# Kernel optimization log

Hardware: AMD Instinct MI355X
Metric: run time of the kernel (lower is better)

Reference implementation:

```python
import jax, jax.numpy as jnp
import numpy as np

RATIOS = np.array([0.5, 1.0, 2.0], np.float32)
SCALES = np.array([8.0, 16.0, 32.0], np.float32)
IMAGE_SIZE = 1920.0
UPPER, LOWER = 0.4, 0.1
NPOS_MAX, NNEG_MAX = 128, 60   # sample_num=256 -> bg_num = min(60, 256-npos) = 60
BETA = 0.1
EPS = 1e-6


def make_anchors(H, W, stride):
    # K = len(RATIOS)*len(SCALES) anchors per grid cell, sizes stride*scale, aspect per ratio
    ws = (stride * SCALES[None, :] * np.sqrt(1.0 / RATIOS[:, None])).reshape(-1)  # [K]
    hs = (stride * SCALES[None, :] * np.sqrt(RATIOS[:, None])).reshape(-1)        # [K]
    cx = (np.arange(W, dtype=np.float32) + 0.5) * stride
    cy = (np.arange(H, dtype=np.float32) + 0.5) * stride
    cxg, cyg = np.meshgrid(cx, cy)  # [H, W]
    a = np.stack([cxg[..., None] - ws / 2, cyg[..., None] - hs / 2,
                  cxg[..., None] + ws / 2, cyg[..., None] + hs / 2], axis=-1)  # [H, W, K, 4]
    return jnp.asarray(a, jnp.float32)


def pairwise_iou(b, g):
    # b: [A, 4], g: [M, 4] -> [A, M]
    ab = jnp.maximum(b[:, 2] - b[:, 0], 0.0) * jnp.maximum(b[:, 3] - b[:, 1], 0.0)
    ag = jnp.maximum(g[:, 2] - g[:, 0], 0.0) * jnp.maximum(g[:, 3] - g[:, 1], 0.0)
    x1 = jnp.maximum(b[:, None, 0], g[None, :, 0])
    y1 = jnp.maximum(b[:, None, 1], g[None, :, 1])
    x2 = jnp.minimum(b[:, None, 2], g[None, :, 2])
    y2 = jnp.minimum(b[:, None, 3], g[None, :, 3])
    inter = jnp.maximum(x2 - x1, 0.0) * jnp.maximum(y2 - y1, 0.0)
    return inter / (ab[:, None] + ag[None, :] - inter + EPS)


def encode(box, anchor):
    # standard (tx, ty, tw, th) box encoding relative to anchor
    aw = anchor[:, 2] - anchor[:, 0]; ah = anchor[:, 3] - anchor[:, 1]
    acx = anchor[:, 0] + 0.5 * aw; acy = anchor[:, 1] + 0.5 * ah
    bw = jnp.maximum(box[:, 2] - box[:, 0], EPS); bh = jnp.maximum(box[:, 3] - box[:, 1], EPS)
    bcx = box[:, 0] + 0.5 * bw; bcy = box[:, 1] + 0.5 * bh
    return jnp.stack([(bcx - acx) / aw, (bcy - acy) / ah,
                      jnp.log(bw / aw), jnp.log(bh / ah)], axis=-1)


def smooth_l1(d):
    ad = jnp.abs(d)
    return jnp.where(ad < BETA, 0.5 * d * d / BETA, ad - 0.5 * BETA)


def per_image(regions, cls, gt, key, anchors_flat, n_norm):
    iou = pairwise_iou(regions, gt)                       # [A, M]
    best = iou.max(axis=1)
    arg = iou.argmax(axis=1).astype(jnp.int32)
    # match(): >= upper -> gt index (positive), < lower -> NEGATIVE(-1), else ignore(-2)
    matches = jnp.where(best >= UPPER, arg, jnp.where(best < LOWER, -1, -2))
    kp, kn = jax.random.split(key)
    # randperm-style sampling without replacement: top_k over random scores on masked anchors
    pos_score = jnp.where(matches >= 0, jax.random.uniform(kp, matches.shape), -1.0)
    pv, pidx = jax.lax.top_k(pos_score, NPOS_MAX)
    pvalid = (pv > 0.0).astype(jnp.float32)               # npos = min(num_pos, 128)
    neg_score = jnp.where(matches == -1, jax.random.uniform(kn, matches.shape), -1.0)
    nv, nidx = jax.lax.top_k(neg_score, NNEG_MAX)
    nvalid = (nv > 0.0).astype(jnp.float32)
    npos = pvalid.sum(); nneg = nvalid.sum()
    lp = cls[pidx]; ln = cls[nidx]
    # BCEWithLogits(mean): label 1 -> softplus(-x), label 0 -> softplus(x)
    bce = jnp.sum(jax.nn.softplus(-lp) * pvalid) + jnp.sum(jax.nn.softplus(ln) * nvalid)
    denom = jnp.maximum(npos + nneg, 1.0)
    cls_loss = bce / denom
    gt_sel = gt[jnp.clip(matches[pidx], 0, gt.shape[0] - 1)]
    anc = anchors_flat[pidx]
    tp = encode(regions[pidx], anc)
    tg = encode(gt_sel, anc)
    l1 = smooth_l1(tp - tg).sum(-1)                       # [NPOS_MAX]
    bbox_loss = jnp.sum(l1 * pvalid) / (jnp.maximum(npos, 1.0) * n_norm)
    pred_mean = (jnp.sum(lp * pvalid) + jnp.sum(ln * nvalid)) / denom
    return cls_loss, bbox_loss, npos, nneg, pred_mean


def reference(cls_scores, bbox_deltas, gt_boxes):
    N, K, H, W = cls_scores.shape
    stride = round(IMAGE_SIZE / W)
    anc = make_anchors(H, W, stride)                      # [H, W, K, 4]
    deltas = bbox_deltas.transpose(0, 2, 3, 1).reshape(N, H, W, K, 4)
    # regions = anchors + deltas, cross_boundary(remove=False) -> clip to image
    regions = jnp.clip(anc[None] + deltas, 0.0, IMAGE_SIZE).reshape(N, -1, 4)
    cls = cls_scores.transpose(0, 2, 3, 1).reshape(N, -1)
    keys = jax.random.split(jax.random.key(42), N)
    cl, bl, fg, bg, pm = jax.vmap(per_image, in_axes=(0, 0, 0, 0, None, None))(
        regions, cls, gt_boxes, keys, anc.reshape(-1, 4), float(N))
    return (cl.sum(), bl.sum(), bg.sum(), fg.sum(), pm[-1])


def setup_inputs():
    key = jax.random.key(0)
    k1, k2, k3, k4 = jax.random.split(key, 4)
    N, K, H, W, M = 8, 9, 120, 120, 64
    cls_scores = jax.random.normal(k1, (N, K, H, W), jnp.float32)
    bbox_deltas = jax.random.normal(k2, (N, 4 * K, H, W), jnp.float32) * 4.0
    xy = jax.random.uniform(k3, (N, M, 2), jnp.float32) * 1500.0
    wh = jax.random.uniform(k4, (N, M, 2), jnp.float32) * 360.0 + 40.0
    gt_boxes = jnp.concatenate([xy, xy + wh], axis=-1)    # valid [x1,y1,x2,y2] in-image
    return {"cls_scores": cls_scores, "bbox_deltas": bbox_deltas, "gt_boxes": gt_boxes}
```

## Files before the change

kernel.cpp:

```cpp
#include <hip/hip_runtime.h>
#include <stdint.h>

#define N_IMG 8
#define K_ANC 9
#define HW_G  14400
#define W_G   120
#define A_TOT 129600
#define M_GT  64
#define NBIN  1024
#define CAP   2048
#define WIN_TOT 2025
#define WPB   4
#define NBLK_M 507
#define NSUB2 64

#define POISON_U32 0xAAAAAAAAu

static constexpr size_t OFF_PHIST = 0;
static constexpr size_t OFF_NHIST = 32768;
static constexpr size_t OFF_CNT   = 65536;
static constexpr size_t OFF_THR   = 65600;
static constexpr size_t OFF_DONE_M= 65792;
static constexpr size_t OFF_DONE  = 65856;
static constexpr size_t OFF_DONE_F= 65888;
static constexpr size_t OFF_ACC   = 65920;
static constexpr size_t OFF_ENT   = 67584;
static constexpr size_t OFF_BND   = OFF_ENT + 4ull * N_IMG * A_TOT;

__device__ __forceinline__ uint32_t rotl32(uint32_t v, int r) {
  return (v << r) | (v >> (32 - r));
}

__device__ void tf2x32(uint32_t k0, uint32_t k1, uint32_t x0, uint32_t x1,
                       uint32_t& o0, uint32_t& o1) {
  uint32_t ks2 = 0x1BD11BDAu ^ k0 ^ k1;
  x0 += k0; x1 += k1;
#define TF_R(r) { x0 += x1; x1 = rotl32(x1, r); x1 ^= x0; }
  TF_R(13) TF_R(15) TF_R(26) TF_R(6)
  x0 += k1; x1 += ks2 + 1u;
  TF_R(17) TF_R(29) TF_R(16) TF_R(24)
  x0 += ks2; x1 += k0 + 2u;
  TF_R(13) TF_R(15) TF_R(26) TF_R(6)
  x0 += k0; x1 += k1 + 3u;
  TF_R(17) TF_R(29) TF_R(16) TF_R(24)
  x0 += k1; x1 += ks2 + 4u;
  TF_R(13) TF_R(15) TF_R(26) TF_R(6)
  x0 += ks2; x1 += k0 + 5u;
#undef TF_R
  o0 = x0; o1 = x1;
}

constexpr uint64_t tf_c(uint32_t k0, uint32_t k1, uint32_t x0, uint32_t x1) {
  const int R[20] = {13,15,26,6,17,29,16,24,13,15,26,6,17,29,16,24,13,15,26,6};
  uint32_t ks[3] = {k0, k1, 0x1BD11BDAu ^ k0 ^ k1};
  x0 += k0; x1 += k1;
  for (int r = 0; r < 20; ++r) {
    x0 += x1; x1 = (x1 << R[r]) | (x1 >> (32 - R[r])); x1 ^= x0;
    if ((r & 3) == 3) {
      int d = r / 4 + 1;
      x0 += ks[d % 3]; x1 += ks[(d + 1) % 3] + (uint32_t)d;
    }
  }
  return ((uint64_t)x0 << 32) | x1;
}

struct KeyTab { uint32_t v[N_IMG][4]; };
constexpr KeyTab make_keys() {
  KeyTab K{};
  for (int n = 0; n < N_IMG; ++n) {
    uint64_t f = tf_c(0u, 42u, 0u, (uint32_t)n);
    uint32_t i0 = (uint32_t)(f >> 32), i1 = (uint32_t)f;
    uint64_t p = tf_c(i0, i1, 0u, 0u);
    uint64_t q = tf_c(i0, i1, 0u, 1u);
    K.v[n][0] = (uint32_t)(p >> 32); K.v[n][1] = (uint32_t)p;
    K.v[n][2] = (uint32_t)(q >> 32); K.v[n][3] = (uint32_t)q;
  }
  return K;
}
__constant__ KeyTab KEYS = make_keys();

__device__ __forceinline__ float rlanef(float v, int l) {
  return __int_as_float(__builtin_amdgcn_readlane(__float_as_int(v), l));
}

__device__ void acc_pos(int n, int l, int m, const float* __restrict__ cls,
                        const float* __restrict__ del, const float* __restrict__ gt,
                        float& sp, float& pr, float& l1s) {
  int k = l / HW_G, hw = l - k * HW_G;
  const float scales[3] = {8.f, 16.f, 32.f};
  const float ratios[3] = {0.5f, 1.f, 2.f};
  float sc = scales[k % 3], rt = ratios[k / 3];
  float wsz = (16.f * sc) * sqrtf(1.f / rt);
  float hsz = (16.f * sc) * sqrtf(rt);
  int w = hw % W_G, h = hw / W_G;
  float cx = ((float)w + 0.5f) * 16.f, cy = ((float)h + 0.5f) * 16.f;
  float ax1 = cx - wsz * 0.5f, ay1 = cy - hsz * 0.5f;
  float ax2 = cx + wsz * 0.5f, ay2 = cy + hsz * 0.5f;
  int base = (n * 36 + k * 4) * HW_G + hw;
  float rx1 = fminf(fmaxf(ax1 + del[base], 0.f), 1920.f);
  float ry1 = fminf(fmaxf(ay1 + del[base + HW_G], 0.f), 1920.f);
  float rx2 = fminf(fmaxf(ax2 + del[base + 2 * HW_G], 0.f), 1920.f);
  float ry2 = fminf(fmaxf(ay2 + del[base + 3 * HW_G], 0.f), 1920.f);
  float L = cls[n * A_TOT + l];
  sp += fmaxf(-L, 0.f) + log1pf(expf(-fabsf(L)));
  pr += L;
  const float* g = gt + (n * M_GT + m) * 4;
  float aw = ax2 - ax1, ah = ay2 - ay1;
  float acx = ax1 + 0.5f * aw, acy = ay1 + 0.5f * ah;
  float bw = fmaxf(rx2 - rx1, 1e-6f), bh = fmaxf(ry2 - ry1, 1e-6f);
  float bcx = rx1 + 0.5f * bw, bcy = ry1 + 0.5f * bh;
  float gw = fmaxf(g[2] - g[0], 1e-6f), gh = fmaxf(g[3] - g[1], 1e-6f);
  float gcx = g[0] + 0.5f * gw, gcy = g[1] + 0.5f * gh;
  float dd[4];
  dd[0] = (bcx - acx) / aw - (gcx - acx) / aw;
  dd[1] = (bcy - acy) / ah - (gcy - acy) / ah;
  dd[2] = logf(bw / aw) - logf(gw / aw);
  dd[3] = logf(bh / ah) - logf(gh / ah);
  float t = 0.f;
  for (int i = 0; i < 4; ++i) {
    float ad = fabsf(dd[i]);
    t += (ad < 0.1f) ? (0.5f * dd[i] * dd[i] / 0.1f) : (ad - 0.05f);
  }
  l1s += t;
}

__device__ void acc_neg(int n, int l, const float* __restrict__ cls,
                        float& sp, float& pr) {
  float L = cls[n * A_TOT + l];
  sp += fmaxf(L, 0.f) + log1pf(expf(-fabsf(L)));
  pr += L;
}

__device__ void reduce3_atomic(float sp, float pr, float l1, float* accf, int n,
                               int tid) {
  __shared__ float swv[3][4];
  float v0 = sp, v1 = pr, v2 = l1;
  for (int off = 32; off > 0; off >>= 1) {
    v0 += __shfl_down(v0, off); v1 += __shfl_down(v1, off); v2 += __shfl_down(v2, off);
  }
  int wv = tid >> 6, ln = tid & 63;
  if (ln == 0) { swv[0][wv] = v0; swv[1][wv] = v1; swv[2][wv] = v2; }
  __syncthreads();
  if (tid == 0) {
    atomicAdd(&accf[n * 48 + 0],  swv[0][0] + swv[0][1] + swv[0][2] + swv[0][3]);
    atomicAdd(&accf[n * 48 + 16], swv[1][0] + swv[1][1] + swv[1][2] + swv[1][3]);
    atomicAdd(&accf[n * 48 + 32], swv[2][0] + swv[2][1] + swv[2][2] + swv[2][3]);
  }
  __syncthreads();
}

__global__ __launch_bounds__(256) void k_match(
    const float* __restrict__ del, const float* __restrict__ gt, uint8_t* ws) {
  const int n = blockIdx.y;
  const int tid = threadIdx.x;
  const int wid = tid >> 6, ln = tid & 63;
  const int win = blockIdx.x * WPB + wid;
  __shared__ int sLast;

  if (win < WIN_TOT) {
    const int k = win / 225;
    const int hw = (win - k * 225) * 64 + ln;

    float4 g4 = reinterpret_cast<const float4*>(gt)[n * M_GT + ln];
    float garea = fmaxf(g4.z - g4.x, 0.f) * fmaxf(g4.w - g4.y, 0.f);

    const float scales[3] = {8.f, 16.f, 32.f};
    const float ratios[3] = {0.5f, 1.f, 2.f};
    float sc = scales[k % 3], rt = ratios[k / 3];
    float wsz = (16.f * sc) * sqrtf(1.f / rt);
    float hsz = (16.f * sc) * sqrtf(rt);
    int w = hw % W_G, h = hw / W_G;
    float cx = ((float)w + 0.5f) * 16.f, cy = ((float)h + 0.5f) * 16.f;
    float ax1 = cx - wsz * 0.5f, ay1 = cy - hsz * 0.5f;
    float ax2 = cx + wsz * 0.5f, ay2 = cy + hsz * 0.5f;
    const float* dp = del + (size_t)(n * 36 + k * 4) * HW_G + hw;
    float rx1 = fminf(fmaxf(ax1 + dp[0], 0.f), 1920.f);
    float ry1 = fminf(fmaxf(ay1 + dp[HW_G], 0.f), 1920.f);
    float rx2 = fminf(fmaxf(ax2 + dp[2 * HW_G], 0.f), 1920.f);
    float ry2 = fminf(fmaxf(ay2 + dp[3 * HW_G], 0.f), 1920.f);
    float ab = fmaxf(rx2 - rx1, 0.f) * fmaxf(ry2 - ry1, 0.f);

    float xmn = rx1, xmx = rx2, ymn = ry1, ymx = ry2;
    for (int off = 32; off > 0; off >>= 1) {
      xmn = fminf(xmn, __shfl_xor(xmn, off));
      xmx = fmaxf(xmx, __shfl_xor(xmx, off));
      ymn = fminf(ymn, __shfl_xor(ymn, off));
      ymx = fmaxf(ymx, __shfl_xor(ymx, off));
    }
    bool keep = (g4.x < xmx) && (g4.z > xmn) && (g4.y < ymx) && (g4.w > ymn);
    unsigned long long mk = __ballot(keep);

    float ib = -1.f, ub = 1.f;
    int arg = 0;
    while (mk) {
      int j = __ffsll((unsigned long long)mk) - 1;
      mk &= mk - 1ull;
      float bx1 = rlanef(g4.x, j), by1 = rlanef(g4.y, j);
      float bx2 = rlanef(g4.z, j), by2 = rlanef(g4.w, j);
      float ga  = rlanef(garea, j);
      float ix1 = fmaxf(rx1, bx1), iy1 = fmaxf(ry1, by1);
      float ix2 = fminf(rx2, bx2), iy2 = fminf(ry2, by2);
      float inter = fmaxf(ix2 - ix1, 0.f) * fmaxf(iy2 - iy1, 0.f);
      float u = ab + ga - inter + 1e-6f;
      bool gc = (inter * ub) > (ib * u);
      ib = gc ? inter : ib;
      ub = gc ? u : ub;
      arg = gc ? j : arg;
    }
    float best = ib / ub;
    int m = (best >= 0.4f) ? arg : ((best < 0.1f) ? -1 : -2);

    uint32_t a32 = (uint32_t)(hw * 9 + k);
    uint32_t sk0 = (m >= 0) ? KEYS.v[n][0] : KEYS.v[n][2];
    uint32_t sk1 = (m >= 0) ? KEYS.v[n][1] : KEYS.v[n][3];
    uint32_t y0, y1;
    tf2x32(sk0, sk1, 0u, a32, y0, y1);
    uint32_t bits = (y0 ^ y1) >> 9;

    uint32_t e = 0u;
    if (bits) {
      if (m >= 0)       e = 0x80000000u | ((uint32_t)m << 23) | bits;
      else if (m == -1) e = bits;
    }
    ((uint32_t*)(ws + OFF_ENT))[(size_t)n * A_TOT + (size_t)k * HW_G + hw] = e;
    if (e) {
      uint32_t* hist = (uint32_t*)(ws + OFF_PHIST);
      uint32_t off = (e >> 31) ? 0u : (uint32_t)(N_IMG * NBIN);
      atomicAdd(&hist[off + n * NBIN + (bits >> 13)], 1u);
    }
  }

  __syncthreads();
  if (tid == 0) {
    uint32_t* dm = (uint32_t*)(ws + OFF_DONE_M);
    sLast = (atomicAdd(&dm[n], 1u) == POISON_U32 + (uint32_t)(NBLK_M - 1)) ? 1 : 0;
  }
  __syncthreads();
  if (sLast && wid < 2) {
    const int s = wid;
    const volatile uint32_t* hb = (const volatile uint32_t*)(ws + OFF_PHIST) +
                                  (s ? (size_t)N_IMG * NBIN : 0) + (size_t)n * NBIN;
    uint32_t hv[16];
    uint32_t ssum = 0u;
#pragma unroll
    for (int i = 0; i < 16; ++i) { hv[i] = hb[ln * 16 + i] - POISON_U32; ssum += hv[i]; }
    uint32_t sfx = ssum;
#pragma unroll
    for (int off = 1; off < 64; off <<= 1) {
      uint32_t v = __shfl_down(sfx, off);
      sfx += (ln + off < 64) ? v : 0u;
    }
    uint32_t total = __shfl(sfx, 0);
    uint32_t ab1 = __shfl_down(sfx, 1);
    uint32_t above = (ln == 63) ? 0u : ab1;
    const uint32_t kk = s ? 60u : 128u;
    int* thr = (int*)(ws + OFF_THR) + n * 6 + s * 3;
    if (total < kk) {
      if (ln == 0) { thr[0] = -1; thr[1] = 0; thr[2] = (int)total; }
    } else if (sfx >= kk && above < kk) {
      uint32_t c = above;
      for (int i = 15;; --i) {
        uint32_t hc = hv[i];
        if (c + hc >= kk) {
          thr[0] = ln * 16 + i; thr[1] = (int)(kk - c); thr[2] = (int)kk;
          break;
        }
        c += hc;
      }
    }
  }
}

__global__ __launch_bounds__(256) void k_scan_bound(
    const float* __restrict__ cls, const float* __restrict__ del,
    const float* __restrict__ gt, float* __restrict__ out, uint8_t* ws) {
  const int sub = blockIdx.x, n = blockIdx.y;
  const int tid = threadIdx.x;
  const uint32_t* ent = (const uint32_t*)(ws + OFF_ENT);
  uint32_t* cnt = (uint32_t*)(ws + OFF_CNT);
  const int* thr = (const int*)(ws + OFF_THR) + n * 6;
  unsigned long long* bnd = (unsigned long long*)(ws + OFF_BND);
  float* accf = (float*)(ws + OFF_ACC);
  uint32_t* done_img = (uint32_t*)(ws + OFF_DONE);
  uint32_t* done_fin = (uint32_t*)(ws + OFF_DONE_F);

  __shared__ unsigned long long sb[CAP];
  __shared__ int sLast, sFin;

  const int bBp = thr[0], bBn = thr[3];
  float sp = 0.f, pr = 0.f, l1 = 0.f;
  const uint32_t* en = ent + (size_t)n * A_TOT;
#pragma unroll
  for (int it = 0; it < 2; ++it) {
    int l0 = sub * 2048 + it * 1024 + tid * 4;
    if (l0 >= A_TOT) continue;
    uint4 e4 = *reinterpret_cast<const uint4*>(en + l0);
    uint32_t ev[4] = {e4.x, e4.y, e4.z, e4.w};
#pragma unroll
    for (int j = 0; j < 4; ++j) {
      uint32_t e = ev[j];
      if (!e) continue;
      bool isPos = (e >> 31) != 0u;
      int bB = isPos ? bBp : bBn;
      int l = l0 + j;
      uint32_t bits = e & 0x7FFFFFu;
      int bin = (int)(bits >> 13);
      if (bin > bB) {
        if (isPos) acc_pos(n, l, (int)((e >> 23) & 0x3Fu), cls, del, gt, sp, pr, l1);
        else       acc_neg(n, l, cls, sp, pr);
      } else if (bin == bB) {
        int wq = isPos ? 0 : 1;
        int i = (int)(atomicAdd(&cnt[n * 2 + wq], 1u) - POISON_U32);
        if (i < CAP) {
          int k = l / HW_G, hw = l - k * HW_G, a = hw * 9 + k;
          unsigned long long rec =
              ((unsigned long long)bits << 17) | (unsigned)(0x1FFFF - a);
          __hip_atomic_store(&bnd[(size_t)(n * 2 + wq) * CAP + i], rec,
                             __ATOMIC_RELAXED, __HIP_MEMORY_SCOPE_AGENT);
        }
      }
    }
  }
  reduce3_atomic(sp, pr, l1, accf, n, tid);

  if (tid == 0)
    sLast = (atomicAdd(&done_img[n], 1u) == POISON_U32 + NSUB2 - 1u) ? 1 : 0;
  __syncthreads();
  if (!sLast) return;

  float sp2 = 0.f, pr2 = 0.f, l12 = 0.f;
  for (int wq = 0; wq < 2; ++wq) {
    int need = thr[wq * 3 + 1];
    if (need > 0) {
      __syncthreads();
      uint32_t cm = __hip_atomic_load(&cnt[n * 2 + wq], __ATOMIC_RELAXED,
                                      __HIP_MEMORY_SCOPE_AGENT);
      int m = min((int)(cm - POISON_U32), CAP);
      unsigned long long* bq = bnd + (size_t)(n * 2 + wq) * CAP;
      for (int i = tid; i < m; i += 256)
        sb[i] = __hip_atomic_load(&bq[i], __ATOMIC_RELAXED,
                                  __HIP_MEMORY_SCOPE_AGENT);
      __syncthreads();
      for (int i = tid; i < m; i += 256) {
        unsigned long long key = sb[i];
        int rank = 0;
        for (int j = 0; j < m; ++j) rank += (sb[j] > key) ? 1 : 0;
        if (rank < need) {
          int a = 0x1FFFF - (int)(key & 0x1FFFFull);
          int k = a % 9, hw = a / 9;
          int l = k * HW_G + hw;
          if (wq == 0) {
            uint32_t e = ent[(size_t)n * A_TOT + l];
            acc_pos(n, l, (int)((e >> 23) & 0x3Fu), cls, del, gt, sp2, pr2, l12);
          } else {
            acc_neg(n, l, cls, sp2, pr2);
          }
        }
      }
      __syncthreads();
    }
  }
  reduce3_atomic(sp2, pr2, l12, accf, n, tid);

  if (tid == 0)
    sFin = (atomicAdd(done_fin, 1u) == POISON_U32 + N_IMG - 1u) ? 1 : 0;
  __syncthreads();
  if (!sFin) return;

  if (tid == 0) {
    const float PF = __uint_as_float(POISON_U32);
    const int* thrr = (const int*)(ws + OFF_THR);
    float c = 0.f, b = 0.f, fg = 0.f, bg = 0.f, pm = 0.f;
    for (int nn = 0; nn < N_IMG; ++nn) {
      float npos = (float)thrr[nn * 6 + 2];
      float nneg = (float)thrr[nn * 6 + 5];
      float denom = fmaxf(npos + nneg, 1.f);
      float a0 = __hip_atomic_load(&accf[nn * 48 + 0],  __ATOMIC_RELAXED,
                                   __HIP_MEMORY_SCOPE_AGENT);
      float a1 = __hip_atomic_load(&accf[nn * 48 + 16], __ATOMIC_RELAXED,
                                   __HIP_MEMORY_SCOPE_AGENT);
      float a2 = __hip_atomic_load(&accf[nn * 48 + 32], __ATOMIC_RELAXED,
                                   __HIP_MEMORY_SCOPE_AGENT);
      c += (a0 - PF) / denom;
      b += (a2 - PF) / (fmaxf(npos, 1.f) * 8.0f);
      fg += npos; bg += nneg;
      if (nn == N_IMG - 1) pm = (a1 - PF) / denom;
    }
    out[0] = c; out[1] = b; out[2] = bg; out[3] = fg; out[4] = pm;
  }
}

extern "C" void kernel_launch(void* const* d_in, const int* in_sizes, int n_in,
                              void* d_out, int out_size, void* d_ws, size_t ws_size,
                              hipStream_t stream) {
  (void)in_sizes; (void)n_in; (void)out_size; (void)ws_size;
  const float* cls = (const float*)d_in[0];
  const float* del = (const float*)d_in[1];
  const float* gt  = (const float*)d_in[2];
  float* out = (float*)d_out;
  uint8_t* ws = (uint8_t*)d_ws;

  hipLaunchKernelGGL(k_match, dim3(NBLK_M, N_IMG), dim3(256), 0, stream,
                     del, gt, ws);
  hipLaunchKernelGGL(k_scan_bound, dim3(NSUB2, N_IMG), dim3(256), 0, stream,
                     cls, del, gt, out, ws);
}
```

Baseline: 144.2 us.

## Split histogram threshold into separate kernel, drop last-block detection in match

The match kernel now runs one wave per 64-anchor window on a 3D grid of 64-thread blocks, with no shared-memory syncs and no atomic done-counter. The per-image threshold search over the histogram moves from the last-finishing block into a new small k_thr kernel launched between match and scan. This removes the block-level barriers and the serial last-block tail, at the cost of an extra kernel launch and many more tiny blocks.

```diff
diff --git a/kernel.cpp b/kernel.cpp
--- a/kernel.cpp
+++ b/kernel.cpp
@@ -9,9 +9,6 @@
 #define M_GT  64
 #define NBIN  1024
 #define CAP   2048
-#define WIN_TOT 2025
-#define WPB   4
-#define NBLK_M 507
 #define NSUB2 64
 
 #define POISON_U32 0xAAAAAAAAu
@@ -20,7 +17,6 @@
 static constexpr size_t OFF_NHIST = 32768;
 static constexpr size_t OFF_CNT   = 65536;
 static constexpr size_t OFF_THR   = 65600;
-static constexpr size_t OFF_DONE_M= 65792;
 static constexpr size_t OFF_DONE  = 65856;
 static constexpr size_t OFF_DONE_F= 65888;
 static constexpr size_t OFF_ACC   = 65920;
@@ -149,124 +145,112 @@
   __syncthreads();
 }
 
-__global__ __launch_bounds__(256) void k_match(
+__global__ __launch_bounds__(64) void k_match(
     const float* __restrict__ del, const float* __restrict__ gt, uint8_t* ws) {
-  const int n = blockIdx.y;
-  const int tid = threadIdx.x;
-  const int wid = tid >> 6, ln = tid & 63;
-  const int win = blockIdx.x * WPB + wid;
-  __shared__ int sLast;
-
-  if (win < WIN_TOT) {
-    const int k = win / 225;
-    const int hw = (win - k * 225) * 64 + ln;
-
-    float4 g4 = reinterpret_cast<const float4*>(gt)[n * M_GT + ln];
-    float garea = fmaxf(g4.z - g4.x, 0.f) * fmaxf(g4.w - g4.y, 0.f);
-
-    const float scales[3] = {8.f, 16.f, 32.f};
-    const float ratios[3] = {0.5f, 1.f, 2.f};
-    float sc = scales[k % 3], rt = ratios[k / 3];
-    float wsz = (16.f * sc) * sqrtf(1.f / rt);
-    float hsz = (16.f * sc) * sqrtf(rt);
-    int w = hw % W_G, h = hw / W_G;
-    float cx = ((float)w + 0.5f) * 16.f, cy = ((float)h + 0.5f) * 16.f;
-    float ax1 = cx - wsz * 0.5f, ay1 = cy - hsz * 0.5f;
-    float ax2 = cx + wsz * 0.5f, ay2 = cy + hsz * 0.5f;
-    const float* dp = del + (size_t)(n * 36 + k * 4) * HW_G + hw;
-    float rx1 = fminf(fmaxf(ax1 + dp[0], 0.f), 1920.f);
-    float ry1 = fminf(fmaxf(ay1 + dp[HW_G], 0.f), 1920.f);
-    float rx2 = fminf(fmaxf(ax2 + dp[2 * HW_G], 0.f), 1920.f);
-    float ry2 = fminf(fmaxf(ay2 + dp[3 * HW_G], 0.f), 1920.f);
-    float ab = fmaxf(rx2 - rx1, 0.f) * fmaxf(ry2 - ry1, 0.f);
-
-    float xmn = rx1, xmx = rx2, ymn = ry1, ymx = ry2;
-    for (int off = 32; off > 0; off >>= 1) {
-      xmn = fminf(xmn, __shfl_xor(xmn, off));
-      xmx = fmaxf(xmx, __shfl_xor(xmx, off));
-      ymn = fminf(ymn, __shfl_xor(ymn, off));
-      ymx = fmaxf(ymx, __shfl_xor(ymx, off));
-    }
-    bool keep = (g4.x < xmx) && (g4.z > xmn) && (g4.y < ymx) && (g4.w > ymn);
-    unsigned long long mk = __ballot(keep);
-
-    float ib = -1.f, ub = 1.f;
-    int arg = 0;
-    while (mk) {
-      int j = __ffsll((unsigned long long)mk) - 1;
-      mk &= mk - 1ull;
-      float bx1 = rlanef(g4.x, j), by1 = rlanef(g4.y, j);
-      float bx2 = rlanef(g4.z, j), by2 = rlanef(g4.w, j);
-      float ga  = rlanef(garea, j);
-      float ix1 = fmaxf(rx1, bx1), iy1 = fmaxf(ry1, by1);
-      float ix2 = fminf(rx2, bx2), iy2 = fminf(ry2, by2);
-      float inter = fmaxf(ix2 - ix1, 0.f) * fmaxf(iy2 - iy1, 0.f);
-      float u = ab + ga - inter + 1e-6f;
-      bool gc = (inter * ub) > (ib * u);
-      ib = gc ? inter : ib;
-      ub = gc ? u : ub;
-      arg = gc ? j : arg;
-    }
-    float best = ib / ub;
-    int m = (best >= 0.4f) ? arg : ((best < 0.1f) ? -1 : -2);
-
-    uint32_t a32 = (uint32_t)(hw * 9 + k);
-    uint32_t sk0 = (m >= 0) ? KEYS.v[n][0] : KEYS.v[n][2];
-    uint32_t sk1 = (m >= 0) ? KEYS.v[n][1] : KEYS.v[n][3];
-    uint32_t y0, y1;
-    tf2x32(sk0, sk1, 0u, a32, y0, y1);
-    uint32_t bits = (y0 ^ y1) >> 9;
-
-    uint32_t e = 0u;
-    if (bits) {
-      if (m >= 0)       e = 0x80000000u | ((uint32_t)m << 23) | bits;
-      else if (m == -1) e = bits;
-    }
-    ((uint32_t*)(ws + OFF_ENT))[(size_t)n * A_TOT + (size_t)k * HW_G + hw] = e;
-    if (e) {
-      uint32_t* hist = (uint32_t*)(ws + OFF_PHIST);
-      uint32_t off = (e >> 31) ? 0u : (uint32_t)(N_IMG * NBIN);
-      atomicAdd(&hist[off + n * NBIN + (bits >> 13)], 1u);
-    }
-  }
-
-  __syncthreads();
-  if (tid == 0) {
-    uint32_t* dm = (uint32_t*)(ws + OFF_DONE_M);
-    sLast = (atomicAdd(&dm[n], 1u) == POISON_U32 + (uint32_t)(NBLK_M - 1)) ? 1 : 0;
-  }
-  __syncthreads();
-  if (sLast && wid < 2) {
-    const int s = wid;
-    const volatile uint32_t* hb = (const volatile uint32_t*)(ws + OFF_PHIST) +
-                                  (s ? (size_t)N_IMG * NBIN : 0) + (size_t)n * NBIN;
-    uint32_t hv[16];
-    uint32_t ssum = 0u;
+  const int k = blockIdx.y, n = blockIdx.z;
+  const int ln = threadIdx.x;
+  const int hw = blockIdx.x * 64 + ln;
+
+  float4 g4 = reinterpret_cast<const float4*>(gt)[n * M_GT + ln];
+  float garea = fmaxf(g4.z - g4.x, 0.f) * fmaxf(g4.w - g4.y, 0.f);
+
+  const float scales[3] = {8.f, 16.f, 32.f};
+  const float ratios[3] = {0.5f, 1.f, 2.f};
+  float sc = scales[k % 3], rt = ratios[k / 3];
+  float wsz = (16.f * sc) * sqrtf(1.f / rt);
+  float hsz = (16.f * sc) * sqrtf(rt);
+  int w = hw % W_G, h = hw / W_G;
+  float cx = ((float)w + 0.5f) * 16.f, cy = ((float)h + 0.5f) * 16.f;
+  float ax1 = cx - wsz * 0.5f, ay1 = cy - hsz * 0.5f;
+  float ax2 = cx + wsz * 0.5f, ay2 = cy + hsz * 0.5f;
+  const float* dp = del + (size_t)(n * 36 + k * 4) * HW_G + hw;
+  float rx1 = fminf(fmaxf(ax1 + dp[0], 0.f), 1920.f);
+  float ry1 = fminf(fmaxf(ay1 + dp[HW_G], 0.f), 1920.f);
+  float rx2 = fminf(fmaxf(ax2 + dp[2 * HW_G], 0.f), 1920.f);
+  float ry2 = fminf(fmaxf(ay2 + dp[3 * HW_G], 0.f), 1920.f);
+  float ab = fmaxf(rx2 - rx1, 0.f) * fmaxf(ry2 - ry1, 0.f);
+
+  float xmn = rx1, xmx = rx2, ymn = ry1, ymx = ry2;
+  for (int off = 32; off > 0; off >>= 1) {
+    xmn = fminf(xmn, __shfl_xor(xmn, off));
+    xmx = fmaxf(xmx, __shfl_xor(xmx, off));
+    ymn = fminf(ymn, __shfl_xor(ymn, off));
+    ymx = fmaxf(ymx, __shfl_xor(ymx, off));
+  }
+  bool keep = (g4.x < xmx) && (g4.z > xmn) && (g4.y < ymx) && (g4.w > ymn);
+  unsigned long long mk = __ballot(keep);
+
+  float ib = -1.f, ub = 1.f;
+  int arg = 0;
+  while (mk) {
+    int j = __ffsll((unsigned long long)mk) - 1;
+    mk &= mk - 1ull;
+    float bx1 = rlanef(g4.x, j), by1 = rlanef(g4.y, j);
+    float bx2 = rlanef(g4.z, j), by2 = rlanef(g4.w, j);
+    float ga  = rlanef(garea, j);
+    float ix1 = fmaxf(rx1, bx1), iy1 = fmaxf(ry1, by1);
+    float ix2 = fminf(rx2, bx2), iy2 = fminf(ry2, by2);
+    float inter = fmaxf(ix2 - ix1, 0.f) * fmaxf(iy2 - iy1, 0.f);
+    float u = ab + ga - inter + 1e-6f;
+    bool gc = (inter * ub) > (ib * u);
+    ib = gc ? inter : ib;
+    ub = gc ? u : ub;
+    arg = gc ? j : arg;
+  }
+  float best = ib / ub;
+  int m = (best >= 0.4f) ? arg : ((best < 0.1f) ? -1 : -2);
+
+  uint32_t a32 = (uint32_t)(hw * 9 + k);
+  uint32_t sk0 = (m >= 0) ? KEYS.v[n][0] : KEYS.v[n][2];
+  uint32_t sk1 = (m >= 0) ? KEYS.v[n][1] : KEYS.v[n][3];
+  uint32_t y0, y1;
+  tf2x32(sk0, sk1, 0u, a32, y0, y1);
+  uint32_t bits = (y0 ^ y1) >> 9;
+
+  uint32_t e = 0u;
+  if (bits) {
+    if (m >= 0)       e = 0x80000000u | ((uint32_t)m << 23) | bits;
+    else if (m == -1) e = bits;
+  }
+  ((uint32_t*)(ws + OFF_ENT))[(size_t)n * A_TOT + (size_t)k * HW_G + hw] = e;
+  if (e) {
+    uint32_t* hist = (uint32_t*)(ws + OFF_PHIST);
+    uint32_t off = (e >> 31) ? 0u : (uint32_t)(N_IMG * NBIN);
+    atomicAdd(&hist[off + n * NBIN + (bits >> 13)], 1u);
+  }
+}
+
+__global__ __launch_bounds__(64) void k_thr(uint8_t* ws) {
+  const int s = blockIdx.x, n = blockIdx.y;
+  const int ln = threadIdx.x;
+  const uint32_t* hb = (const uint32_t*)(ws + OFF_PHIST) +
+                       (s ? (size_t)N_IMG * NBIN : 0) + (size_t)n * NBIN;
+  uint32_t hv[16];
+  uint32_t ssum = 0u;
 #pragma unroll
-    for (int i = 0; i < 16; ++i) { hv[i] = hb[ln * 16 + i] - POISON_U32; ssum += hv[i]; }
-    uint32_t sfx = ssum;
+  for (int i = 0; i < 16; ++i) { hv[i] = hb[ln * 16 + i] - POISON_U32; ssum += hv[i]; }
+  uint32_t sfx = ssum;
 #pragma unroll
-    for (int off = 1; off < 64; off <<= 1) {
-      uint32_t v = __shfl_down(sfx, off);
-      sfx += (ln + off < 64) ? v : 0u;
-    }
-    uint32_t total = __shfl(sfx, 0);
-    uint32_t ab1 = __shfl_down(sfx, 1);
-    uint32_t above = (ln == 63) ? 0u : ab1;
-    const uint32_t kk = s ? 60u : 128u;
-    int* thr = (int*)(ws + OFF_THR) + n * 6 + s * 3;
-    if (total < kk) {
-      if (ln == 0) { thr[0] = -1; thr[1] = 0; thr[2] = (int)total; }
-    } else if (sfx >= kk && above < kk) {
-      uint32_t c = above;
-      for (int i = 15;; --i) {
-        uint32_t hc = hv[i];
-        if (c + hc >= kk) {
-          thr[0] = ln * 16 + i; thr[1] = (int)(kk - c); thr[2] = (int)kk;
-          break;
-        }
-        c += hc;
+  for (int off = 1; off < 64; off <<= 1) {
+    uint32_t v = __shfl_down(sfx, off);
+    sfx += (ln + off < 64) ? v : 0u;
+  }
+  uint32_t total = __shfl(sfx, 0);
+  uint32_t ab1 = __shfl_down(sfx, 1);
+  uint32_t above = (ln == 63) ? 0u : ab1;
+  const uint32_t kk = s ? 60u : 128u;
+  int* thr = (int*)(ws + OFF_THR) + n * 6 + s * 3;
+  if (total < kk) {
+    if (ln == 0) { thr[0] = -1; thr[1] = 0; thr[2] = (int)total; }
+  } else if (sfx >= kk && above < kk) {
+    uint32_t c = above;
+    for (int i = 15;; --i) {
+      uint32_t hc = hv[i];
+      if (c + hc >= kk) {
+        thr[0] = ln * 16 + i; thr[1] = (int)(kk - c); thr[2] = (int)kk;
+        break;
       }
+      c += hc;
     }
   }
 }
@@ -400,8 +384,9 @@
   float* out = (float*)d_out;
   uint8_t* ws = (uint8_t*)d_ws;
 
-  hipLaunchKernelGGL(k_match, dim3(NBLK_M, N_IMG), dim3(256), 0, stream,
+  hipLaunchKernelGGL(k_match, dim3(HW_G / 64, K_ANC, N_IMG), dim3(64), 0, stream,
                      del, gt, ws);
+  hipLaunchKernelGGL(k_thr, dim3(2, N_IMG), dim3(64), 0, stream, ws);
   hipLaunchKernelGGL(k_scan_bound, dim3(NSUB2, N_IMG), dim3(256), 0, stream,
                      cls, del, gt, out, ws);
 }
```

New measurement: 124.8 us. 13.5% less time.

## Move histogram threshold selection from last match block into every scan block

Applied to the files above, without the earlier changes.

Removes the last-block-done atomic counter and threshold computation from the match kernel. Each scan block now recomputes the per-image histogram threshold itself and keeps the result in shared memory. Only block 0 writes the positive and negative counts to global memory for the final reduction. Match blocks shrink to 128 threads with twice as many blocks, which drops the tail serialization at the cost of redundant histogram reads in 64 blocks per image.

```diff
diff --git a/kernel.cpp b/kernel.cpp
--- a/kernel.cpp
+++ b/kernel.cpp
@@ -10,8 +10,7 @@
 #define NBIN  1024
 #define CAP   2048
 #define WIN_TOT 2025
-#define WPB   4
-#define NBLK_M 507
+#define NBLK_M 1013
 #define NSUB2 64
 
 #define POISON_U32 0xAAAAAAAAu
@@ -20,7 +19,6 @@
 static constexpr size_t OFF_NHIST = 32768;
 static constexpr size_t OFF_CNT   = 65536;
 static constexpr size_t OFF_THR   = 65600;
-static constexpr size_t OFF_DONE_M= 65792;
 static constexpr size_t OFF_DONE  = 65856;
 static constexpr size_t OFF_DONE_F= 65888;
 static constexpr size_t OFF_ACC   = 65920;
@@ -149,125 +147,82 @@
   __syncthreads();
 }
 
-__global__ __launch_bounds__(256) void k_match(
+__global__ __launch_bounds__(128) void k_match(
     const float* __restrict__ del, const float* __restrict__ gt, uint8_t* ws) {
   const int n = blockIdx.y;
   const int tid = threadIdx.x;
-  const int wid = tid >> 6, ln = tid & 63;
-  const int win = blockIdx.x * WPB + wid;
-  __shared__ int sLast;
-
-  if (win < WIN_TOT) {
-    const int k = win / 225;
-    const int hw = (win - k * 225) * 64 + ln;
-
-    float4 g4 = reinterpret_cast<const float4*>(gt)[n * M_GT + ln];
-    float garea = fmaxf(g4.z - g4.x, 0.f) * fmaxf(g4.w - g4.y, 0.f);
-
-    const float scales[3] = {8.f, 16.f, 32.f};
-    const float ratios[3] = {0.5f, 1.f, 2.f};
-    float sc = scales[k % 3], rt = ratios[k / 3];
-    float wsz = (16.f * sc) * sqrtf(1.f / rt);
-    float hsz = (16.f * sc) * sqrtf(rt);
-    int w = hw % W_G, h = hw / W_G;
-    float cx = ((float)w + 0.5f) * 16.f, cy = ((float)h + 0.5f) * 16.f;
-    float ax1 = cx - wsz * 0.5f, ay1 = cy - hsz * 0.5f;
-    float ax2 = cx + wsz * 0.5f, ay2 = cy + hsz * 0.5f;
-    const float* dp = del + (size_t)(n * 36 + k * 4) * HW_G + hw;
-    float rx1 = fminf(fmaxf(ax1 + dp[0], 0.f), 1920.f);
-    float ry1 = fminf(fmaxf(ay1 + dp[HW_G], 0.f), 1920.f);
-    float rx2 = fminf(fmaxf(ax2 + dp[2 * HW_G], 0.f), 1920.f);
-    float ry2 = fminf(fmaxf(ay2 + dp[3 * HW_G], 0.f), 1920.f);
-    float ab = fmaxf(rx2 - rx1, 0.f) * fmaxf(ry2 - ry1, 0.f);
-
-    float xmn = rx1, xmx = rx2, ymn = ry1, ymx = ry2;
-    for (int off = 32; off > 0; off >>= 1) {
-      xmn = fminf(xmn, __shfl_xor(xmn, off));
-      xmx = fmaxf(xmx, __shfl_xor(xmx, off));
-      ymn = fminf(ymn, __shfl_xor(ymn, off));
-      ymx = fmaxf(ymx, __shfl_xor(ymx, off));
-    }
-    bool keep = (g4.x < xmx) && (g4.z > xmn) && (g4.y < ymx) && (g4.w > ymn);
-    unsigned long long mk = __ballot(keep);
-
-    float ib = -1.f, ub = 1.f;
-    int arg = 0;
-    while (mk) {
-      int j = __ffsll((unsigned long long)mk) - 1;
-      mk &= mk - 1ull;
-      float bx1 = rlanef(g4.x, j), by1 = rlanef(g4.y, j);
-      float bx2 = rlanef(g4.z, j), by2 = rlanef(g4.w, j);
-      float ga  = rlanef(garea, j);
-      float ix1 = fmaxf(rx1, bx1), iy1 = fmaxf(ry1, by1);
-      float ix2 = fminf(rx2, bx2), iy2 = fminf(ry2, by2);
-      float inter = fmaxf(ix2 - ix1, 0.f) * fmaxf(iy2 - iy1, 0.f);
-      float u = ab + ga - inter + 1e-6f;
-      bool gc = (inter * ub) > (ib * u);
-      ib = gc ? inter : ib;
-      ub = gc ? u : ub;
-      arg = gc ? j : arg;
-    }
-    float best = ib / ub;
-    int m = (best >= 0.4f) ? arg : ((best < 0.1f) ? -1 : -2);
-
-    uint32_t a32 = (uint32_t)(hw * 9 + k);
-    uint32_t sk0 = (m >= 0) ? KEYS.v[n][0] : KEYS.v[n][2];
-    uint32_t sk1 = (m >= 0) ? KEYS.v[n][1] : KEYS.v[n][3];
-    uint32_t y0, y1;
-    tf2x32(sk0, sk1, 0u, a32, y0, y1);
-    uint32_t bits = (y0 ^ y1) >> 9;
-
-    uint32_t e = 0u;
-    if (bits) {
-      if (m >= 0)       e = 0x80000000u | ((uint32_t)m << 23) | bits;
-      else if (m == -1) e = bits;
-    }
-    ((uint32_t*)(ws + OFF_ENT))[(size_t)n * A_TOT + (size_t)k * HW_G + hw] = e;
-    if (e) {
-      uint32_t* hist = (uint32_t*)(ws + OFF_PHIST);
-      uint32_t off = (e >> 31) ? 0u : (uint32_t)(N_IMG * NBIN);
-      atomicAdd(&hist[off + n * NBIN + (bits >> 13)], 1u);
-    }
-  }
-
-  __syncthreads();
-  if (tid == 0) {
-    uint32_t* dm = (uint32_t*)(ws + OFF_DONE_M);
-    sLast = (atomicAdd(&dm[n], 1u) == POISON_U32 + (uint32_t)(NBLK_M - 1)) ? 1 : 0;
-  }
-  __syncthreads();
-  if (sLast && wid < 2) {
-    const int s = wid;
-    const volatile uint32_t* hb = (const volatile uint32_t*)(ws + OFF_PHIST) +
-                                  (s ? (size_t)N_IMG * NBIN : 0) + (size_t)n * NBIN;
-    uint32_t hv[16];
-    uint32_t ssum = 0u;
-#pragma unroll
-    for (int i = 0; i < 16; ++i) { hv[i] = hb[ln * 16 + i] - POISON_U32; ssum += hv[i]; }
-    uint32_t sfx = ssum;
-#pragma unroll
-    for (int off = 1; off < 64; off <<= 1) {
-      uint32_t v = __shfl_down(sfx, off);
-      sfx += (ln + off < 64) ? v : 0u;
-    }
-    uint32_t total = __shfl(sfx, 0);
-    uint32_t ab1 = __shfl_down(sfx, 1);
-    uint32_t above = (ln == 63) ? 0u : ab1;
-    const uint32_t kk = s ? 60u : 128u;
-    int* thr = (int*)(ws + OFF_THR) + n * 6 + s * 3;
-    if (total < kk) {
-      if (ln == 0) { thr[0] = -1; thr[1] = 0; thr[2] = (int)total; }
-    } else if (sfx >= kk && above < kk) {
-      uint32_t c = above;
-      for (int i = 15;; --i) {
-        uint32_t hc = hv[i];
-        if (c + hc >= kk) {
-          thr[0] = ln * 16 + i; thr[1] = (int)(kk - c); thr[2] = (int)kk;
-          break;
-        }
-        c += hc;
-      }
-    }
+  const int ln = tid & 63;
+  const int win = blockIdx.x * 2 + (tid >> 6);
+  if (win >= WIN_TOT) return;
+  const int k = win / 225;
+  const int hw = (win - k * 225) * 64 + ln;
+
+  float4 g4 = reinterpret_cast<const float4*>(gt)[n * M_GT + ln];
+  float garea = fmaxf(g4.z - g4.x, 0.f) * fmaxf(g4.w - g4.y, 0.f);
+
+  const float scales[3] = {8.f, 16.f, 32.f};
+  const float ratios[3] = {0.5f, 1.f, 2.f};
+  float sc = scales[k % 3], rt = ratios[k / 3];
+  float wsz = (16.f * sc) * sqrtf(1.f / rt);
+  float hsz = (16.f * sc) * sqrtf(rt);
+  int w = hw % W_G, h = hw / W_G;
+  float cx = ((float)w + 0.5f) * 16.f, cy = ((float)h + 0.5f) * 16.f;
+  float ax1 = cx - wsz * 0.5f, ay1 = cy - hsz * 0.5f;
+  float ax2 = cx + wsz * 0.5f, ay2 = cy + hsz * 0.5f;
+  const float* dp = del + (size_t)(n * 36 + k * 4) * HW_G + hw;
+  float rx1 = fminf(fmaxf(ax1 + dp[0], 0.f), 1920.f);
+  float ry1 = fminf(fmaxf(ay1 + dp[HW_G], 0.f), 1920.f);
+  float rx2 = fminf(fmaxf(ax2 + dp[2 * HW_G], 0.f), 1920.f);
+  float ry2 = fminf(fmaxf(ay2 + dp[3 * HW_G], 0.f), 1920.f);
+  float ab = fmaxf(rx2 - rx1, 0.f) * fmaxf(ry2 - ry1, 0.f);
+
+  float xmn = rx1, xmx = rx2, ymn = ry1, ymx = ry2;
+  for (int off = 32; off > 0; off >>= 1) {
+    xmn = fminf(xmn, __shfl_xor(xmn, off));
+    xmx = fmaxf(xmx, __shfl_xor(xmx, off));
+    ymn = fminf(ymn, __shfl_xor(ymn, off));
+    ymx = fmaxf(ymx, __shfl_xor(ymx, off));
+  }
+  bool keep = (g4.x < xmx) && (g4.z > xmn) && (g4.y < ymx) && (g4.w > ymn);
+  unsigned long long mk = __ballot(keep);
+
+  float ib = -1.f, ub = 1.f;
+  int arg = 0;
+  while (mk) {
+    int j = __ffsll((unsigned long long)mk) - 1;
+    mk &= mk - 1ull;
+    float bx1 = rlanef(g4.x, j), by1 = rlanef(g4.y, j);
+    float bx2 = rlanef(g4.z, j), by2 = rlanef(g4.w, j);
+    float ga  = rlanef(garea, j);
+    float ix1 = fmaxf(rx1, bx1), iy1 = fmaxf(ry1, by1);
+    float ix2 = fminf(rx2, bx2), iy2 = fminf(ry2, by2);
+    float inter = fmaxf(ix2 - ix1, 0.f) * fmaxf(iy2 - iy1, 0.f);
+    float u = ab + ga - inter + 1e-6f;
+    bool gc = (inter * ub) > (ib * u);
+    ib = gc ? inter : ib;
+    ub = gc ? u : ub;
+    arg = gc ? j : arg;
+  }
+  float best = ib / ub;
+  int m = (best >= 0.4f) ? arg : ((best < 0.1f) ? -1 : -2);
+
+  uint32_t a32 = (uint32_t)(hw * 9 + k);
+  uint32_t sk0 = (m >= 0) ? KEYS.v[n][0] : KEYS.v[n][2];
+  uint32_t sk1 = (m >= 0) ? KEYS.v[n][1] : KEYS.v[n][3];
+  uint32_t y0, y1;
+  tf2x32(sk0, sk1, 0u, a32, y0, y1);
+  uint32_t bits = (y0 ^ y1) >> 9;
+
+  uint32_t e = 0u;
+  if (bits) {
+    if (m >= 0)       e = 0x80000000u | ((uint32_t)m << 23) | bits;
+    else if (m == -1) e = bits;
+  }
+  ((uint32_t*)(ws + OFF_ENT))[(size_t)n * A_TOT + (size_t)k * HW_G + hw] = e;
+  if (e) {
+    uint32_t* hist = (uint32_t*)(ws + OFF_PHIST);
+    uint32_t off = (e >> 31) ? 0u : (uint32_t)(N_IMG * NBIN);
+    atomicAdd(&hist[off + n * NBIN + (bits >> 13)], 1u);
   }
 }
 
@@ -278,16 +233,62 @@
   const int tid = threadIdx.x;
   const uint32_t* ent = (const uint32_t*)(ws + OFF_ENT);
   uint32_t* cnt = (uint32_t*)(ws + OFF_CNT);
-  const int* thr = (const int*)(ws + OFF_THR) + n * 6;
+  int* thrg = (int*)(ws + OFF_THR);
   unsigned long long* bnd = (unsigned long long*)(ws + OFF_BND);
   float* accf = (float*)(ws + OFF_ACC);
   uint32_t* done_img = (uint32_t*)(ws + OFF_DONE);
   uint32_t* done_fin = (uint32_t*)(ws + OFF_DONE_F);
 
   __shared__ unsigned long long sb[CAP];
+  __shared__ int tb[2][3];
   __shared__ int sLast, sFin;
 
-  const int bBp = thr[0], bBn = thr[3];
+  {
+    const int wid = tid >> 6, ln = tid & 63;
+    if (wid < 2) {
+      const int s = wid;
+      const uint32_t* hb = (const uint32_t*)(ws + OFF_PHIST) +
+                           (s ? (size_t)N_IMG * NBIN : 0) + (size_t)n * NBIN;
+      uint32_t hv[16];
+      uint32_t ssum = 0u;
+#pragma unroll
+      for (int i = 0; i < 16; ++i) {
+        hv[i] = hb[ln * 16 + i] - POISON_U32; ssum += hv[i];
+      }
+      uint32_t sfx = ssum;
+#pragma unroll
+      for (int off = 1; off < 64; off <<= 1) {
+        uint32_t v = __shfl_down(sfx, off);
+        sfx += (ln + off < 64) ? v : 0u;
+      }
+      uint32_t total = __shfl(sfx, 0);
+      uint32_t ab1 = __shfl_down(sfx, 1);
+      uint32_t above = (ln == 63) ? 0u : ab1;
+      const uint32_t kk = s ? 60u : 128u;
+      if (total < kk) {
+        if (ln == 0) { tb[s][0] = -1; tb[s][1] = 0; tb[s][2] = (int)total; }
+      } else if (sfx >= kk && above < kk) {
+        uint32_t c = above;
+        for (int i = 15;; --i) {
+          uint32_t hc = hv[i];
+          if (c + hc >= kk) {
+            tb[s][0] = ln * 16 + i; tb[s][1] = (int)(kk - c); tb[s][2] = (int)kk;
+            break;
+          }
+          c += hc;
+        }
+      }
+    }
+    __syncthreads();
+  }
+  if (sub == 0 && tid == 0) {
+    __hip_atomic_store(&thrg[n * 2 + 0], tb[0][2], __ATOMIC_RELAXED,
+                       __HIP_MEMORY_SCOPE_AGENT);
+    __hip_atomic_store(&thrg[n * 2 + 1], tb[1][2], __ATOMIC_RELAXED,
+                       __HIP_MEMORY_SCOPE_AGENT);
+  }
+
+  const int bBp = tb[0][0], bBn = tb[1][0];
   float sp = 0.f, pr = 0.f, l1 = 0.f;
   const uint32_t* en = ent + (size_t)n * A_TOT;
 #pragma unroll
@@ -330,7 +331,7 @@
 
   float sp2 = 0.f, pr2 = 0.f, l12 = 0.f;
   for (int wq = 0; wq < 2; ++wq) {
-    int need = thr[wq * 3 + 1];
+    int need = tb[wq][1];
     if (need > 0) {
       __syncthreads();
       uint32_t cm = __hip_atomic_load(&cnt[n * 2 + wq], __ATOMIC_RELAXED,
@@ -369,11 +370,12 @@
 
   if (tid == 0) {
     const float PF = __uint_as_float(POISON_U32);
-    const int* thrr = (const int*)(ws + OFF_THR);
     float c = 0.f, b = 0.f, fg = 0.f, bg = 0.f, pm = 0.f;
     for (int nn = 0; nn < N_IMG; ++nn) {
-      float npos = (float)thrr[nn * 6 + 2];
-      float nneg = (float)thrr[nn * 6 + 5];
+      float npos = (float)__hip_atomic_load(&thrg[nn * 2 + 0], __ATOMIC_RELAXED,
+                                            __HIP_MEMORY_SCOPE_AGENT);
+      float nneg = (float)__hip_atomic_load(&thrg[nn * 2 + 1], __ATOMIC_RELAXED,
+                                            __HIP_MEMORY_SCOPE_AGENT);
       float denom = fmaxf(npos + nneg, 1.f);
       float a0 = __hip_atomic_load(&accf[nn * 48 + 0],  __ATOMIC_RELAXED,
                                    __HIP_MEMORY_SCOPE_AGENT);
@@ -400,7 +402,7 @@
   float* out = (float*)d_out;
   uint8_t* ws = (uint8_t*)d_ws;
 
-  hipLaunchKernelGGL(k_match, dim3(NBLK_M, N_IMG), dim3(256), 0, stream,
+  hipLaunchKernelGGL(k_match, dim3(NBLK_M, N_IMG), dim3(128), 0, stream,
                      del, gt, ws);
   hipLaunchKernelGGL(k_scan_bound, dim3(NSUB2, N_IMG), dim3(256), 0, stream,
                      cls, del, gt, out, ws);
```

Result: faster. 125.6 us (-12.9%).
